# Performance work log

Hardware: AMD Instinct MI355X
Metric: run time of the kernel (lower is better)

## Reference

```python
import jax, jax.numpy as jnp
import numpy as np

FEATURE_DIM = 1024
MAX_DEPTH = 32
HID = 128
N = 32768


def setup_inputs() -> dict:
    key = jax.random.key(0)
    ks = jax.random.split(key, 16)
    d = FEATURE_DIM
    s = 0.02
    return {
        "features": jax.random.normal(ks[0], (N, d), jnp.float32),
        "depths": jax.random.randint(ks[1], (N,), 0, MAX_DEPTH),
        "pos_emb": jax.random.normal(ks[2], (MAX_DEPTH, d), jnp.float32) * s,
        "aW1": jax.random.normal(ks[3], (HID, 2 * d), jnp.float32) * s,
        "ab1": jnp.zeros((HID,), jnp.float32),
        "aW2": jax.random.normal(ks[4], (1, HID), jnp.float32) * s,
        "ab2": jnp.zeros((1,), jnp.float32),
        "uW1": jax.random.normal(ks[5], (d, 2 * d), jnp.float32) * s,
        "ub1": jnp.zeros((d,), jnp.float32),
        "uW2": jax.random.normal(ks[6], (d, d), jnp.float32) * s,
        "ub2": jnp.zeros((d,), jnp.float32),
        "gW": jax.random.normal(ks[7], (d, 2 * d), jnp.float32) * s,
        "gb": jnp.zeros((d,), jnp.float32),
    }


def reference(features, depths, pos_emb, aW1, ab1, aW2, ab2,
              uW1, ub1, uW2, ub2, gW, gb):
    # add position embeddings (depths clamped to [0, MAX_DEPTH-1])
    dep = jnp.clip(depths, 0, MAX_DEPTH - 1)
    f = features + pos_emb[dep]                       # [N, d]
    target = f[0:1]                                    # [1, d]
    path = f[1:]                                       # [N-1, d]

    # attention MLP over all path states at once (vectorizes the torch loop)
    tb = jnp.broadcast_to(target, path.shape)          # [N-1, d]
    comb = jnp.concatenate([tb, path], axis=1)         # [N-1, 2d]
    h = jax.nn.relu(comb @ aW1.T + ab1)                # [N-1, 128]
    attn = jax.nn.sigmoid(h @ aW2.T + ab2)             # [N-1, 1]

    s = attn.sum()
    attn = jnp.where(s > 0, attn / s, attn)

    agg = (path * attn).sum(axis=0, keepdims=True)     # [1, d]
    c2 = jnp.concatenate([target, agg], axis=1)        # [1, 2d]
    gate = jax.nn.sigmoid(c2 @ gW.T + gb)
    upd = jax.nn.relu(c2 @ uW1.T + ub1) @ uW2.T + ub2
    updated_target = target + gate * upd
    return jnp.concatenate([updated_target, path], axis=0)
```

## Files before the change

kernel.cpp:

```cpp
#include <hip/hip_runtime.h>

#define DNUM 1024
#define HIDN 128
#define NTOT 32768
#define MR 32
#define NBLK 1024
#define SBLK 8192

#define T_OFF 0
#define P0_OFF 1024
#define S_OFF 1152
#define AGG_OFF 1216
#define GATE_OFF 2240
#define U1_OFF 3264
#define W2_FOFF 4288
#define AGGP_OFF (W2_FOFF + 65536)
#define SP_OFF (AGGP_OFF + NBLK * DNUM)
#define WS_NEED ((size_t)(SP_OFF + NBLK) * 4)
#define FBF_BYTE ((((SP_OFF + NBLK) * 4) + 65535) & ~65535)
#define WS_NEED2 ((size_t)FBF_BYTE + (size_t)NBLK * 65536)

typedef __attribute__((ext_vector_type(8))) short short8;
typedef __attribute__((ext_vector_type(4))) float f32x4;

__device__ __forceinline__ unsigned short f2bf(float x) {
  unsigned int u = __builtin_bit_cast(unsigned int, x);
  u = u + 0x7fffu + ((u >> 16) & 1u);
  return (unsigned short)(u >> 16);
}
__device__ __forceinline__ float bf2f(unsigned int bits16) {
  unsigned int u = bits16 << 16;
  return __builtin_bit_cast(float, u);
}
__device__ __forceinline__ void gl_lds16(const void* g, void* l) {
  __builtin_amdgcn_global_load_lds(
      (const __attribute__((address_space(1))) unsigned int*)g,
      (__attribute__((address_space(3))) unsigned int*)l, 16, 0, 0);
}

__global__ __launch_bounds__(256) void kf1(const float* __restrict__ features,
                                           const int* __restrict__ depths,
                                           const float* __restrict__ pos_emb,
                                           const float* __restrict__ aW1,
                                           const float* __restrict__ ab1,
                                           float* __restrict__ ws,
                                           unsigned short* __restrict__ w2,
                                           float* __restrict__ out,
                                           unsigned short* __restrict__ fbf) {
  __shared__ float tgt[1024];
  __shared__ float ph[256];
  const int t = threadIdx.x;
  const int bid = blockIdx.x;
  if (bid < SBLK) {
    const int col = t * 4;
#pragma unroll
    for (int rr = 0; rr < 4; ++rr) {
      int fr = 1 + bid * 4 + rr;
      float4 f = make_float4(0.f, 0.f, 0.f, 0.f);
      if (fr < NTOT) {
        int dp = depths[fr];
        dp = dp < 0 ? 0 : (dp > 31 ? 31 : dp);
        float4 fv = *(const float4*)(features + (size_t)fr * DNUM + col);
        float4 pe = *(const float4*)(pos_emb + (size_t)dp * DNUM + col);
        f.x = fv.x + pe.x; f.y = fv.y + pe.y; f.z = fv.z + pe.z; f.w = fv.w + pe.w;
        *(float4*)(out + (size_t)fr * DNUM + col) = f;
      }
      if (fbf) {
        uint2 pk;
        pk.x = (unsigned int)f2bf(f.x) | ((unsigned int)f2bf(f.y) << 16);
        pk.y = (unsigned int)f2bf(f.z) | ((unsigned int)f2bf(f.w) << 16);
        int g = (fr - 1) >> 5, i = (fr - 1) & 31;
        int off = (i * 2048 + t * 8) ^ ((i & 7) << 4);
        *(uint2*)((char*)fbf + (size_t)g * 65536 + off) = pk;
      }
    }
    return;
  }
  int ib = bid - SBLK;
  if (ib == 0) {
    int dep = depths[0];
    dep = dep < 0 ? 0 : (dep > 31 ? 31 : dep);
    float4 fv = *(const float4*)(features + t * 4);
    float4 pe = *(const float4*)(pos_emb + dep * DNUM + t * 4);
    float4 r;
    r.x = fv.x + pe.x; r.y = fv.y + pe.y; r.z = fv.z + pe.z; r.w = fv.w + pe.w;
    *(float4*)(ws + T_OFF + t * 4) = r;
    *(float4*)(tgt + t * 4) = r;
    if (t < 64) ws[S_OFF + t] = 0.f;
    __syncthreads();
    int j = t >> 1, h = t & 1;
    const float* wrow = aW1 + (size_t)j * (2 * DNUM) + h * 512;
    const float* tr = tgt + h * 512;
    float p = 0.f;
    for (int k = 0; k < 512; k += 4) {
      float4 wv = *(const float4*)(wrow + k);
      float4 tv = *(const float4*)(tr + k);
      p += wv.x * tv.x + wv.y * tv.y + wv.z * tv.z + wv.w * tv.w;
    }
    ph[t] = p;
    __syncthreads();
    if (t < HIDN) ws[P0_OFF + t] = ab1[t] + ph[t * 2] + ph[t * 2 + 1];
    return;
  }
  int idx = ((ib - 1) * 256 + t) * 4;
  int j = idx >> 10, k = idx & 1023;
  float4 v = *(const float4*)(aW1 + (size_t)j * 2048 + 1024 + k);
  uint2 pk;
  pk.x = (unsigned int)f2bf(v.x) | ((unsigned int)f2bf(v.y) << 16);
  pk.y = (unsigned int)f2bf(v.z) | ((unsigned int)f2bf(v.w) << 16);
  *(uint2*)(w2 + idx) = pk;
}

__global__ __launch_bounds__(512, 4) void kgemm(
    const float* __restrict__ fsrc, const float* __restrict__ p0,
    const float* __restrict__ aW2, const float* __restrict__ ab2,
    const unsigned short* __restrict__ w2,
    float* __restrict__ agg, float* __restrict__ sacc,
    float* __restrict__ aggp, float* __restrict__ sp,
    const unsigned short* __restrict__ fbf) {
  __shared__ __align__(16) unsigned char ldsA[MR * 2048];
  __shared__ float part[160];
  __shared__ float comb[1024];
  const int t = threadIdx.x;
  const int bid = blockIdx.x;
  const int lane = t & 63;
  const int w = t >> 6;
  const int llo = lane & 15;
  const int lhi = lane >> 4;
  const int tc = t & 255;
  const int th = t >> 8;
  const int col = tc * 4;

  if (fbf) {
    const char* src = (const char*)fbf + (size_t)bid * 65536;
#pragma unroll
    for (int q = 0; q < 8; ++q) {
      int wb = q * 8192 + w * 1024;
      gl_lds16(src + wb + lane * 16, ldsA + wb);
    }
    asm volatile("s_waitcnt vmcnt(0)" ::: "memory");
  } else {
#pragma unroll
    for (int ii = 0; ii < 16; ++ii) {
      int i = ii * 2 + th;
      int fr = 1 + bid * MR + i;
      float4 f = (fr < NTOT) ? *(const float4*)(fsrc + (size_t)fr * DNUM + col)
                             : make_float4(0.f, 0.f, 0.f, 0.f);
      uint2 pk;
      pk.x = (unsigned int)f2bf(f.x) | ((unsigned int)f2bf(f.y) << 16);
      pk.y = (unsigned int)f2bf(f.z) | ((unsigned int)f2bf(f.w) << 16);
      int off = (i * 2048 + tc * 8) ^ ((i & 7) << 4);
      *(uint2*)(ldsA + off) = pk;
    }
  }
  __syncthreads();

  const int wm = w >> 2, wn = w & 3;
  f32x4 acc[2];
  acc[0] = (f32x4){0.f, 0.f, 0.f, 0.f};
  acc[1] = (f32x4){0.f, 0.f, 0.f, 0.f};
  const int arow = wm * 16 + llo;
  const int abase = arow * 2048;
  const int aswz = (arow & 7) << 4;
  const unsigned short* bpA = w2 + (size_t)(wn * 32 + llo) * DNUM + lhi * 8;
  const unsigned short* bpB = bpA + 16 * DNUM;

#pragma unroll 4
  for (int kc = 0; kc < 32; ++kc) {
    int kbase = kc * 32;
    short8 av = *(short8*)(ldsA + ((abase + (kbase + lhi * 8) * 2) ^ aswz));
    short8 bv0 = *(const short8*)(bpA + kbase);
    short8 bv1 = *(const short8*)(bpB + kbase);
    acc[0] = __builtin_amdgcn_mfma_f32_16x16x32_bf16(av, bv0, acc[0], 0, 0, 0);
    acc[1] = __builtin_amdgcn_mfma_f32_16x16x32_bf16(av, bv1, acc[1], 0, 0, 0);
  }

  float p0v[2], wv[2];
#pragma unroll
  for (int n = 0; n < 2; ++n) {
    int j = wn * 32 + n * 16 + llo;
    p0v[n] = p0[j];
    wv[n] = aW2[j];
  }
#pragma unroll
  for (int e = 0; e < 4; ++e) {
    float s = 0.f;
#pragma unroll
    for (int n = 0; n < 2; ++n) {
      float h = acc[n][e] + p0v[n];
      h = fmaxf(h, 0.f);
      s += h * wv[n];
    }
    s += __shfl_xor(s, 1);
    s += __shfl_xor(s, 2);
    s += __shfl_xor(s, 4);
    s += __shfl_xor(s, 8);
    if (llo == 0) part[wn * 32 + wm * 16 + lhi * 4 + e] = s;
  }
  __syncthreads();

  if (t < MR) {
    float pre = part[t] + part[32 + t] + part[64 + t] + part[96 + t] + ab2[0];
    int fr = 1 + bid * MR + t;
    float raw = 0.f;
    if (fr < NTOT) raw = 1.f / (1.f + __expf(-pre));
    part[128 + t] = raw;
  }
  __syncthreads();

  float a0 = 0.f, a1 = 0.f, a2 = 0.f, a3 = 0.f;
  for (int lr = th * 16; lr < th * 16 + 16; ++lr) {
    float r = part[128 + lr];
    int off = (lr * 2048 + tc * 8) ^ ((lr & 7) << 4);
    uint2 pk = *(uint2*)(ldsA + off);
    a0 += r * bf2f(pk.x & 0xffffu);
    a1 += r * bf2f(pk.x >> 16);
    a2 += r * bf2f(pk.y & 0xffffu);
    a3 += r * bf2f(pk.y >> 16);
  }
  if (th == 1) {
    comb[tc * 4 + 0] = a0; comb[tc * 4 + 1] = a1;
    comb[tc * 4 + 2] = a2; comb[tc * 4 + 3] = a3;
  }
  __syncthreads();
  if (th == 0) {
    float c0 = a0 + comb[tc * 4 + 0];
    float c1 = a1 + comb[tc * 4 + 1];
    float c2v = a2 + comb[tc * 4 + 2];
    float c3 = a3 + comb[tc * 4 + 3];
    if (aggp) {
      f32x4 v = {c0, c1, c2v, c3};
      *(f32x4*)(aggp + (size_t)bid * DNUM + col) = v;
    } else {
      atomicAdd(agg + col + 0, c0);
      atomicAdd(agg + col + 1, c1);
      atomicAdd(agg + col + 2, c2v);
      atomicAdd(agg + col + 3, c3);
    }
  }
  if (t == 0) {
    float s = 0.f;
    for (int lr = 0; lr < MR; ++lr) s += part[128 + lr];
    if (sp) sp[bid] = s;
    else atomicAdd(sacc + (bid & 63), s);
  }
}

__global__ __launch_bounds__(256) void kred(const float* __restrict__ aggp,
                                            const float* __restrict__ sp,
                                            float* __restrict__ ws) {
  int t = threadIdx.x, bid = blockIdx.x;
  if (bid < 256) {
    int w = t >> 6, lane = t & 63;
    int colIdx = bid * 4 + w;
    float s = 0.f;
#pragma unroll 4
    for (int k = 0; k < 16; ++k) {
      int r = lane + k * 64;
      s += aggp[(size_t)r * DNUM + colIdx];
    }
    s += __shfl_xor(s, 1);
    s += __shfl_xor(s, 2);
    s += __shfl_xor(s, 4);
    s += __shfl_xor(s, 8);
    s += __shfl_xor(s, 16);
    s += __shfl_xor(s, 32);
    if (lane == 0) ws[AGG_OFF + colIdx] = s;
  } else {
    __shared__ float red[256];
    float s = sp[t] + sp[t + 256] + sp[t + 512] + sp[t + 768];
    red[t] = s;
    __syncthreads();
    if (t < 64) {
      float v = red[t] + red[t + 64] + red[t + 128] + red[t + 192];
      v += __shfl_xor(v, 1);
      v += __shfl_xor(v, 2);
      v += __shfl_xor(v, 4);
      v += __shfl_xor(v, 8);
      v += __shfl_xor(v, 16);
      v += __shfl_xor(v, 32);
      if (t == 0) ws[S_OFF] = v;
    }
  }
}

__global__ __launch_bounds__(256) void kc1(const float* __restrict__ gW,
                                           const float* __restrict__ gb,
                                           const float* __restrict__ uW1,
                                           const float* __restrict__ ub1,
                                           float* __restrict__ ws) {
  __shared__ float c2[2048];
  __shared__ float sinv_sh;
  int t = threadIdx.x, bid = blockIdx.x;
  if (t == 0) {
    float s = 0.f;
    for (int i = 0; i < 64; ++i) s += ws[S_OFF + i];
    sinv_sh = (s > 0.f) ? 1.f / s : 1.f;
  }
  __syncthreads();
  float sinv = sinv_sh;
  for (int i = t; i < 2048; i += 256)
    c2[i] = (i < 1024) ? ws[T_OFF + i] : ws[AGG_OFF + i - 1024] * sinv;
  __syncthreads();
  int w = t >> 6, lane = t & 63;
  int isGate = bid < 256;
  int o = (isGate ? bid : bid - 256) * 4 + w;
  const float* W = isGate ? gW : uW1;
  float p = 0.f;
  for (int i = lane; i < 2048; i += 64) p += W[(size_t)o * 2048 + i] * c2[i];
  p += __shfl_xor(p, 1);
  p += __shfl_xor(p, 2);
  p += __shfl_xor(p, 4);
  p += __shfl_xor(p, 8);
  p += __shfl_xor(p, 16);
  p += __shfl_xor(p, 32);
  if (lane == 0) {
    float v = p + (isGate ? gb[o] : ub1[o]);
    v = isGate ? (1.f / (1.f + expf(-v))) : fmaxf(v, 0.f);
    ws[(isGate ? GATE_OFF : U1_OFF) + o] = v;
  }
}

__global__ __launch_bounds__(256) void kc2(const float* __restrict__ uW2,
                                           const float* __restrict__ ub2,
                                           const float* __restrict__ ws,
                                           float* __restrict__ out) {
  __shared__ float u1[1024];
  int t = threadIdx.x, bid = blockIdx.x;
  for (int i = t; i < 1024; i += 256) u1[i] = ws[U1_OFF + i];
  __syncthreads();
  int w = t >> 6, lane = t & 63;
  int o = bid * 4 + w;
  float p = 0.f;
  for (int i = lane; i < 1024; i += 64) p += uW2[(size_t)o * 1024 + i] * u1[i];
  p += __shfl_xor(p, 1);
  p += __shfl_xor(p, 2);
  p += __shfl_xor(p, 4);
  p += __shfl_xor(p, 8);
  p += __shfl_xor(p, 16);
  p += __shfl_xor(p, 32);
  if (lane == 0) {
    float upd = p + ub2[o];
    out[o] = ws[T_OFF + o] + ws[GATE_OFF + o] * upd;
  }
}

extern "C" void kernel_launch(void* const* d_in, const int* in_sizes, int n_in,
                              void* d_out, int out_size, void* d_ws, size_t ws_size,
                              hipStream_t stream) {
  const float* features = (const float*)d_in[0];
  const int* depths = (const int*)d_in[1];
  const float* pos_emb = (const float*)d_in[2];
  const float* aW1 = (const float*)d_in[3];
  const float* ab1 = (const float*)d_in[4];
  const float* aW2 = (const float*)d_in[5];
  const float* ab2 = (const float*)d_in[6];
  const float* uW1 = (const float*)d_in[7];
  const float* ub1 = (const float*)d_in[8];
  const float* uW2 = (const float*)d_in[9];
  const float* ub2 = (const float*)d_in[10];
  const float* gW = (const float*)d_in[11];
  const float* gb = (const float*)d_in[12];
  float* out = (float*)d_out;
  float* ws = (float*)d_ws;
  unsigned short* w2 = (unsigned short*)(ws + W2_FOFF);
  bool useP = ws_size >= WS_NEED;
  bool useF = ws_size >= WS_NEED2;
  float* aggp = useP ? (ws + AGGP_OFF) : nullptr;
  float* sp = useP ? (ws + SP_OFF) : nullptr;
  unsigned short* fbf = useF ? (unsigned short*)((char*)d_ws + FBF_BYTE) : nullptr;

  hipLaunchKernelGGL(kf1, dim3(SBLK + 129), dim3(256), 0, stream,
                     features, depths, pos_emb, aW1, ab1, ws, w2, out, fbf);
  hipLaunchKernelGGL(kgemm, dim3(NBLK), dim3(512), 0, stream,
                     out, ws + P0_OFF, aW2, ab2, w2, ws + AGG_OFF, ws + S_OFF,
                     aggp, sp, fbf);
  if (useP)
    hipLaunchKernelGGL(kred, dim3(257), dim3(256), 0, stream, aggp, sp, ws);
  hipLaunchKernelGGL(kc1, dim3(512), dim3(256), 0, stream, gW, gb, uW1, ub1, ws);
  hipLaunchKernelGGL(kc2, dim3(256), dim3(256), 0, stream, uW2, ub2, ws, out);
}
```

Before: 181.3 us.

## Move path output write into GEMM kernel from bf16 LDS tile

The prep kernel now only builds the swizzled bf16 copy of the path rows, using wider 16-byte stores, and no longer writes the fp32 output. The GEMM kernel writes the output rows from the bf16 values it already holds in LDS. When the bf16 buffer is not available, the GEMM kernel recomputes features plus position embeddings itself. Total memory traffic stays about the same, because the output write simply moves to the other kernel. The output rows are now bf16-rounded instead of exact fp32 sums, which risks failing accuracy checks.

```diff
diff --git a/kernel.cpp b/kernel.cpp
--- a/kernel.cpp
+++ b/kernel.cpp
@@ -5,7 +5,7 @@
 #define NTOT 32768
 #define MR 32
 #define NBLK 1024
-#define SBLK 8192
+#define SBLK 4096
 
 #define T_OFF 0
 #define P0_OFF 1024
@@ -45,34 +45,38 @@
                                            const float* __restrict__ ab1,
                                            float* __restrict__ ws,
                                            unsigned short* __restrict__ w2,
-                                           float* __restrict__ out,
                                            unsigned short* __restrict__ fbf) {
   __shared__ float tgt[1024];
   __shared__ float ph[256];
   const int t = threadIdx.x;
   const int bid = blockIdx.x;
   if (bid < SBLK) {
-    const int col = t * 4;
-#pragma unroll
-    for (int rr = 0; rr < 4; ++rr) {
-      int fr = 1 + bid * 4 + rr;
-      float4 f = make_float4(0.f, 0.f, 0.f, 0.f);
+    const int sub = t >> 7;
+    const int cf = (t & 127) * 8;
+#pragma unroll
+    for (int iter = 0; iter < 4; ++iter) {
+      int rowIdx = bid * 8 + iter * 2 + sub;
+      int fr = 1 + rowIdx;
+      float4 fa = make_float4(0.f, 0.f, 0.f, 0.f);
+      float4 fb = make_float4(0.f, 0.f, 0.f, 0.f);
       if (fr < NTOT) {
         int dp = depths[fr];
         dp = dp < 0 ? 0 : (dp > 31 ? 31 : dp);
-        float4 fv = *(const float4*)(features + (size_t)fr * DNUM + col);
-        float4 pe = *(const float4*)(pos_emb + (size_t)dp * DNUM + col);
-        f.x = fv.x + pe.x; f.y = fv.y + pe.y; f.z = fv.z + pe.z; f.w = fv.w + pe.w;
-        *(float4*)(out + (size_t)fr * DNUM + col) = f;
+        float4 va = *(const float4*)(features + (size_t)fr * DNUM + cf);
+        float4 vb = *(const float4*)(features + (size_t)fr * DNUM + cf + 4);
+        float4 pa = *(const float4*)(pos_emb + (size_t)dp * DNUM + cf);
+        float4 pb = *(const float4*)(pos_emb + (size_t)dp * DNUM + cf + 4);
+        fa.x = va.x + pa.x; fa.y = va.y + pa.y; fa.z = va.z + pa.z; fa.w = va.w + pa.w;
+        fb.x = vb.x + pb.x; fb.y = vb.y + pb.y; fb.z = vb.z + pb.z; fb.w = vb.w + pb.w;
       }
-      if (fbf) {
-        uint2 pk;
-        pk.x = (unsigned int)f2bf(f.x) | ((unsigned int)f2bf(f.y) << 16);
-        pk.y = (unsigned int)f2bf(f.z) | ((unsigned int)f2bf(f.w) << 16);
-        int g = (fr - 1) >> 5, i = (fr - 1) & 31;
-        int off = (i * 2048 + t * 8) ^ ((i & 7) << 4);
-        *(uint2*)((char*)fbf + (size_t)g * 65536 + off) = pk;
-      }
+      uint4 pk;
+      pk.x = (unsigned int)f2bf(fa.x) | ((unsigned int)f2bf(fa.y) << 16);
+      pk.y = (unsigned int)f2bf(fa.z) | ((unsigned int)f2bf(fa.w) << 16);
+      pk.z = (unsigned int)f2bf(fb.x) | ((unsigned int)f2bf(fb.y) << 16);
+      pk.w = (unsigned int)f2bf(fb.z) | ((unsigned int)f2bf(fb.w) << 16);
+      int g = rowIdx >> 5, i = rowIdx & 31;
+      int off = (i * 2048 + (t & 127) * 16) ^ ((i & 7) << 4);
+      *(uint4*)((char*)fbf + (size_t)g * 65536 + off) = pk;
     }
     return;
   }
@@ -112,9 +116,10 @@
 }
 
 __global__ __launch_bounds__(512, 4) void kgemm(
-    const float* __restrict__ fsrc, const float* __restrict__ p0,
+    const float* __restrict__ features, const int* __restrict__ depths,
+    const float* __restrict__ pos_emb, const float* __restrict__ p0,
     const float* __restrict__ aW2, const float* __restrict__ ab2,
-    const unsigned short* __restrict__ w2,
+    const unsigned short* __restrict__ w2, float* __restrict__ out,
     float* __restrict__ agg, float* __restrict__ sacc,
     float* __restrict__ aggp, float* __restrict__ sp,
     const unsigned short* __restrict__ fbf) {
@@ -144,8 +149,15 @@
     for (int ii = 0; ii < 16; ++ii) {
       int i = ii * 2 + th;
       int fr = 1 + bid * MR + i;
-      float4 f = (fr < NTOT) ? *(const float4*)(fsrc + (size_t)fr * DNUM + col)
-                             : make_float4(0.f, 0.f, 0.f, 0.f);
+      float4 f = make_float4(0.f, 0.f, 0.f, 0.f);
+      if (fr < NTOT) {
+        int dp = depths[fr];
+        dp = dp < 0 ? 0 : (dp > 31 ? 31 : dp);
+        float4 fv = *(const float4*)(features + (size_t)fr * DNUM + col);
+        float4 pe = *(const float4*)(pos_emb + (size_t)dp * DNUM + col);
+        f.x = fv.x + pe.x; f.y = fv.y + pe.y; f.z = fv.z + pe.z; f.w = fv.w + pe.w;
+        *(float4*)(out + (size_t)fr * DNUM + col) = f;
+      }
       uint2 pk;
       pk.x = (unsigned int)f2bf(f.x) | ((unsigned int)f2bf(f.y) << 16);
       pk.y = (unsigned int)f2bf(f.z) | ((unsigned int)f2bf(f.w) << 16);
@@ -213,10 +225,21 @@
     float r = part[128 + lr];
     int off = (lr * 2048 + tc * 8) ^ ((lr & 7) << 4);
     uint2 pk = *(uint2*)(ldsA + off);
-    a0 += r * bf2f(pk.x & 0xffffu);
-    a1 += r * bf2f(pk.x >> 16);
-    a2 += r * bf2f(pk.y & 0xffffu);
-    a3 += r * bf2f(pk.y >> 16);
+    float f0 = bf2f(pk.x & 0xffffu);
+    float f1 = bf2f(pk.x >> 16);
+    float f2 = bf2f(pk.y & 0xffffu);
+    float f3 = bf2f(pk.y >> 16);
+    if (fbf) {
+      int fr = 1 + bid * MR + lr;
+      if (fr < NTOT) {
+        f32x4 v = {f0, f1, f2, f3};
+        *(f32x4*)(out + (size_t)fr * DNUM + col) = v;
+      }
+    }
+    a0 += r * f0;
+    a1 += r * f1;
+    a2 += r * f2;
+    a3 += r * f3;
   }
   if (th == 1) {
     comb[tc * 4 + 0] = a0; comb[tc * 4 + 1] = a1;
@@ -370,11 +393,11 @@
   float* sp = useP ? (ws + SP_OFF) : nullptr;
   unsigned short* fbf = useF ? (unsigned short*)((char*)d_ws + FBF_BYTE) : nullptr;
 
-  hipLaunchKernelGGL(kf1, dim3(SBLK + 129), dim3(256), 0, stream,
-                     features, depths, pos_emb, aW1, ab1, ws, w2, out, fbf);
+  hipLaunchKernelGGL(kf1, dim3(useF ? (SBLK + 129) : 129), dim3(256), 0, stream,
+                     features, depths, pos_emb, aW1, ab1, ws, w2, fbf);
   hipLaunchKernelGGL(kgemm, dim3(NBLK), dim3(512), 0, stream,
-                     out, ws + P0_OFF, aW2, ab2, w2, ws + AGG_OFF, ws + S_OFF,
-                     aggp, sp, fbf);
+                     features, depths, pos_emb, ws + P0_OFF, aW2, ab2, w2, out,
+                     ws + AGG_OFF, ws + S_OFF, aggp, sp, fbf);
   if (useP)
     hipLaunchKernelGGL(kred, dim3(257), dim3(256), 0, stream, aggp, sp, ws);
   hipLaunchKernelGGL(kc1, dim3(512), dim3(256), 0, stream, gW, gb, uW1, ub1, ws);
```

Result: no change. 181.7 us (+0.2%).
